# Optimization experiments

Hardware: AMD Instinct MI355X
Metric: run time of the kernel (lower is better)

The kernel has to match this reference:

```python
import jax, jax.numpy as jnp
import numpy as np

B, N, IN_DIM, DIM, KNN = 8, 2048, 128, 128, 16
POS_H = 64
ATTN_H = DIM * 4
EPS = 1e-5
SCALE = 1.0 / np.sqrt(DIM).astype(np.float32)


def setup_inputs() -> dict:
    key = jax.random.key(0)
    ks = jax.random.split(key, 10)
    nrm = lambda k, shape, s=0.02: jax.random.normal(k, shape, jnp.float32) * s
    return dict(
        ori_x=jax.random.normal(ks[0], (B, N, IN_DIM), jnp.float32),
        pos=jax.random.normal(ks[1], (B, N, 3), jnp.float32),
        w_in=nrm(ks[2], (IN_DIM, DIM)),
        w_qkv=nrm(ks[3], (DIM, 3 * DIM)),
        w_out=nrm(ks[4], (DIM, IN_DIM)),
        pos_w1=nrm(ks[5], (3, POS_H)), pos_b1=jnp.zeros((POS_H,), jnp.float32),
        pos_bn_g=jnp.ones((POS_H,), jnp.float32), pos_bn_b=jnp.zeros((POS_H,), jnp.float32),
        pos_bn_m=jnp.zeros((POS_H,), jnp.float32), pos_bn_v=jnp.ones((POS_H,), jnp.float32),
        pos_w2=nrm(ks[6], (POS_H, DIM)), pos_b2=jnp.zeros((DIM,), jnp.float32),
        attn_w1=nrm(ks[7], (DIM, ATTN_H)), attn_b1=jnp.zeros((ATTN_H,), jnp.float32),
        attn_bn_g=jnp.ones((ATTN_H,), jnp.float32), attn_bn_b=jnp.zeros((ATTN_H,), jnp.float32),
        attn_bn_m=jnp.zeros((ATTN_H,), jnp.float32), attn_bn_v=jnp.ones((ATTN_H,), jnp.float32),
        attn_w2=nrm(ks[8], (ATTN_H, DIM)), attn_b2=jnp.zeros((DIM,), jnp.float32),
    )


def _bn_eval(x, g, b, m, v):
    # BatchNorm2d in eval mode; channel is the last axis in our [b,n,k,C] layout
    return (x - m) * (g * jax.lax.rsqrt(v + EPS)) + b


def reference(ori_x, pos, w_in, w_qkv, w_out,
              pos_w1, pos_b1, pos_bn_g, pos_bn_b, pos_bn_m, pos_bn_v, pos_w2, pos_b2,
              attn_w1, attn_b1, attn_bn_g, attn_bn_b, attn_bn_m, attn_bn_v, attn_w2, attn_b2):
    x = ori_x @ w_in                                  # [b,n,dim]
    qkv = x @ w_qkv
    q, k, v = jnp.split(qkv, 3, axis=-1)              # each [b,n,dim]

    # pairwise squared distances [b,n,n] (monotone in rel_dist -> same topk)
    sq = jnp.sum(pos * pos, axis=-1)
    d2 = sq[:, :, None] + sq[:, None, :] - 2.0 * jnp.einsum('bnd,bmd->bnm', pos, pos)
    _, idx = jax.lax.top_k(-d2, KNN)                  # [b,n,KNN] nearest neighbors

    gather = jax.vmap(lambda t, i: t[i])              # [n,C],[n,k] -> [n,k,C] per batch
    k_g = gather(k, idx)                              # [b,n,k,dim]
    v_g = gather(v, idx)
    pos_g = gather(pos, idx)                          # [b,n,k,3]

    rel_pos = pos[:, :, None, :] - pos_g              # [b,n,k,3]
    pe = jax.nn.relu(_bn_eval(rel_pos @ pos_w1 + pos_b1, pos_bn_g, pos_bn_b, pos_bn_m, pos_bn_v))
    pe = pe @ pos_w2 + pos_b2                         # [b,n,k,dim]

    qk_rel = q[:, :, None, :] - k_g                   # [b,n,k,dim]
    h = jax.nn.relu(_bn_eval((qk_rel + pe) @ attn_w1 + attn_b1,
                             attn_bn_g, attn_bn_b, attn_bn_m, attn_bn_v))
    h = h @ attn_w2 + attn_b2                         # [b,n,k,dim]

    attn = jax.nn.softmax(h * SCALE, axis=-2)         # softmax over neighbors
    agg = jnp.sum(attn * (v_g + pe), axis=2)          # [b,n,dim]
    return agg @ w_out + ori_x
```

## Files before the change

kernel.cpp:

```cpp
#include <hip/hip_runtime.h>

#define EPS 1e-5f

constexpr int NB   = 8;
constexpr int NN   = 2048;
constexpr int DIM  = 128;
constexpr int KNN  = 16;
constexpr int AH   = 512;
constexpr int NPTS = NB * NN;
constexpr float SCALE = 0.08838834764831845f;

typedef __attribute__((ext_vector_type(8))) short short8;
typedef __attribute__((ext_vector_type(4))) float floatx4;

__device__ __forceinline__ short f2bf(float f) {
  union { float f; unsigned u; } a; a.f = f;
  return (short)((a.u + 0x8000u) >> 16);
}
__device__ __forceinline__ float bf2f(short s) {
  union { unsigned u; float f; } a; a.u = ((unsigned)(unsigned short)s) << 16;
  return a.f;
}

__global__ __launch_bounds__(256) void gemm_f32(
    const float* __restrict__ A, const float* __restrict__ W,
    float* __restrict__ C, int M, int N, int K)
{
  __shared__ float As[64][33];
  __shared__ float Ws[32][65];
  const int bm = blockIdx.x * 64, bn = blockIdx.y * 64;
  const int tid = threadIdx.x;
  const int tx = tid & 15, ty = tid >> 4;
  float acc[4][4] = {};
  for (int k0 = 0; k0 < K; k0 += 32) {
#pragma unroll
    for (int i = 0; i < 8; ++i) {
      int e = tid + i * 256;
      As[e >> 5][e & 31] = A[(size_t)(bm + (e >> 5)) * K + k0 + (e & 31)];
    }
#pragma unroll
    for (int i = 0; i < 8; ++i) {
      int e = tid + i * 256;
      Ws[e >> 6][e & 63] = W[(size_t)(k0 + (e >> 6)) * N + bn + (e & 63)];
    }
    __syncthreads();
#pragma unroll
    for (int kk = 0; kk < 32; ++kk) {
      float a[4], w[4];
#pragma unroll
      for (int i = 0; i < 4; ++i) a[i] = As[ty * 4 + i][kk];
#pragma unroll
      for (int j = 0; j < 4; ++j) w[j] = Ws[kk][tx * 4 + j];
#pragma unroll
      for (int i = 0; i < 4; ++i)
#pragma unroll
        for (int j = 0; j < 4; ++j)
          acc[i][j] += a[i] * w[j];
    }
    __syncthreads();
  }
#pragma unroll
  for (int i = 0; i < 4; ++i)
#pragma unroll
    for (int j = 0; j < 4; ++j)
      C[(size_t)(bm + ty * 4 + i) * N + bn + tx * 4 + j] = acc[i][j];
}

__global__ __launch_bounds__(256) void knn_kernel(
    const float* __restrict__ pos_t, int* __restrict__ idx_out)
{
  const int tid = threadIdx.x;
  const int lane = tid & 63;
  const int p = blockIdx.x * 4 + (tid >> 6);
  const int b = p >> 11, i = p & (NN - 1);
  const float* px = pos_t + (size_t)b * 3 * NN;
  const float* py = px + NN;
  const float* pz = py + NN;
  const float xi = px[i], yi = py[i], zi = pz[i];
  const float sqi = xi * xi + yi * yi + zi * zi;
  float v[32];
#pragma unroll
  for (int t = 0; t < 32; ++t) {
    int j = t * 64 + lane;
    float xj = px[j], yj = py[j], zj = pz[j];
    float sqj = xj * xj + yj * yj + zj * zj;
    float dot = xi * xj + yi * yj + zi * zj;
    v[t] = sqi + sqj - 2.0f * dot;
  }
  for (int s = 0; s < KNN; ++s) {
    float bv = 3.4e38f; int bj = 1 << 30;
#pragma unroll
    for (int t = 0; t < 32; ++t) {
      if (v[t] < bv) { bv = v[t]; bj = t * 64 + lane; }
    }
#pragma unroll
    for (int m = 1; m < 64; m <<= 1) {
      float ov = __shfl_xor(bv, m);
      int   oj = __shfl_xor(bj, m);
      if (ov < bv || (ov == bv && oj < bj)) { bv = ov; bj = oj; }
    }
    if (lane == 0) idx_out[(size_t)p * KNN + s] = bj;
#pragma unroll
    for (int t = 0; t < 32; ++t)
      if (bj == t * 64 + lane) v[t] = 3.4e38f;
  }
}

__global__ __launch_bounds__(256) void pack_weights(
    const float* __restrict__ attn_w1, const float* __restrict__ attn_w2,
    const float* __restrict__ pos_w2, const float* __restrict__ Wf,
    const float* __restrict__ w_out, const float* __restrict__ pos,
    const float* __restrict__ attn_b1, const float* __restrict__ abn_g,
    const float* __restrict__ abn_b, const float* __restrict__ abn_m,
    const float* __restrict__ abn_v,
    const float* __restrict__ pos_b1, const float* __restrict__ pbn_g,
    const float* __restrict__ pbn_b, const float* __restrict__ pbn_m,
    const float* __restrict__ pbn_v, const float* __restrict__ pos_b2,
    short* __restrict__ w1p, short* __restrict__ w2p, short* __restrict__ pw2p,
    short* __restrict__ wfp, short* __restrict__ wop,
    float* __restrict__ biasq,
    float* __restrict__ t1sc, float* __restrict__ t1bi,
    float* __restrict__ phsc, float* __restrict__ phbi,
    float* __restrict__ pos_t)
{
  int t = blockIdx.x * 256 + threadIdx.x;
  if (t < 65536) {
    int j = t & 7, lane = (t >> 3) & 63, ks = (t >> 9) & 3, nt = (t >> 11) & 3, ch = t >> 13;
    int q = lane >> 4, cc = lane & 15;
    int k = ks * 32 + q * 8 + j, n = ch * 64 + nt * 16 + cc;
    w1p[t] = f2bf(attn_w1[(size_t)k * AH + n]);
  } else if (t < 131072) {
    int e = t - 65536;
    int j = e & 7, lane = (e >> 3) & 63, ks = (e >> 9) & 1, nt = (e >> 10) & 7, ch = e >> 13;
    int q = lane >> 4, cc = lane & 15;
    int k = ch * 64 + ks * 32 + q * 8 + j, n = nt * 16 + cc;
    w2p[e] = f2bf(attn_w2[(size_t)k * DIM + n]);
  } else if (t < 139264) {
    int e = t - 131072;
    int j = e & 7, lane = (e >> 3) & 63, ks = (e >> 9) & 1, nt = e >> 10;
    int q = lane >> 4, cc = lane & 15;
    int k = ks * 32 + q * 8 + j, n = nt * 16 + cc;
    pw2p[e] = f2bf(pos_w2[(size_t)k * DIM + n]);
  } else if (t < 188416) {
    int e = t - 139264;
    int j = e & 7, lane = (e >> 3) & 63, ks = (e >> 9) & 3, nt = (e >> 11) & 7, nc = e >> 14;
    int q = lane >> 4, cc = lane & 15;
    int k = ks * 32 + q * 8 + j, n = nc * 128 + nt * 16 + cc;
    wfp[e] = f2bf(Wf[(size_t)k * 384 + n]);
  } else if (t < 204800) {
    int e = t - 188416;
    int j = e & 7, lane = (e >> 3) & 63, ks = (e >> 9) & 3, nt = (e >> 11) & 7;
    int q = lane >> 4, cc = lane & 15;
    int k = ks * 32 + q * 8 + j, n = nt * 16 + cc;
    wop[e] = f2bf(w_out[(size_t)k * DIM + n]);
  } else if (t < 205184) {
    int c = t - 204800;
    biasq[c] = (c < 128) ? pos_b2[c] : ((c < 256) ? 0.0f : pos_b2[c - 256]);
  } else if (t < 205696) {
    int c = t - 205184;
    t1sc[c] = abn_g[c] * rsqrtf(abn_v[c] + EPS);
  } else if (t < 206208) {
    int c = t - 205696;
    float sc = abn_g[c] * rsqrtf(abn_v[c] + EPS);
    t1bi[c] = (attn_b1[c] - abn_m[c]) * sc + abn_b[c];
  } else if (t < 206272) {
    int c = t - 206208;
    phsc[c] = pbn_g[c] * rsqrtf(pbn_v[c] + EPS);
  } else if (t < 206336) {
    int c = t - 206272;
    float sc = pbn_g[c] * rsqrtf(pbn_v[c] + EPS);
    phbi[c] = (pos_b1[c] - pbn_m[c]) * sc + pbn_b[c];
  } else if (t < 206336 + NPTS * 3) {
    int e = t - 206336;
    int p = e / 3, d = e - p * 3;
    int b = p >> 11, n = p & (NN - 1);
    pos_t[((size_t)b * 3 + d) * NN + n] = pos[e];
  }
}

__global__ __launch_bounds__(256, 4) void gemm_in(
    const float* __restrict__ A, const short* __restrict__ wfp,
    const float* __restrict__ biasq, short* __restrict__ C)
{
  __shared__ short As[64 * 128];
  const int tid = threadIdx.x;
  const int lane = tid & 63, w = tid >> 6;
  const int wr = w >> 1, wc = w & 1;
  const int q = lane >> 4, cc = lane & 15;
  const int row0 = blockIdx.x * 64;
#pragma unroll
  for (int it = 0; it < 4; ++it) {
    int e = tid + it * 256;
    int row = e >> 4, cg = e & 15;
    const float* src = A + (size_t)(row0 + row) * 128 + cg * 8;
    float4 f0 = *(const float4*)src, f1 = *(const float4*)(src + 4);
    short8 v;
    v[0] = f2bf(f0.x); v[1] = f2bf(f0.y); v[2] = f2bf(f0.z); v[3] = f2bf(f0.w);
    v[4] = f2bf(f1.x); v[5] = f2bf(f1.y); v[6] = f2bf(f1.z); v[7] = f2bf(f1.w);
    *(short8*)(As + row * 128 + ((cg ^ (row & 15)) << 3)) = v;
  }
  __syncthreads();
  for (int nc = 0; nc < 3; ++nc) {
    floatx4 acc[2][4];
#pragma unroll
    for (int i = 0; i < 2; ++i)
#pragma unroll
      for (int jt = 0; jt < 4; ++jt) acc[i][jt] = (floatx4){0.f, 0.f, 0.f, 0.f};
#pragma unroll
    for (int ks = 0; ks < 4; ++ks) {
      short8 a8[2], b8[4];
#pragma unroll
      for (int i = 0; i < 2; ++i) {
        int row = (wr * 2 + i) * 16 + cc;
        a8[i] = *(const short8*)(As + row * 128 + (((ks * 4 + q) ^ cc) << 3));
      }
#pragma unroll
      for (int jt = 0; jt < 4; ++jt)
        b8[jt] = *(const short8*)(wfp + ((((nc * 8 + wc * 4 + jt) * 4 + ks) * 64 + lane) << 3));
#pragma unroll
      for (int i = 0; i < 2; ++i)
#pragma unroll
        for (int jt = 0; jt < 4; ++jt)
          acc[i][jt] = __builtin_amdgcn_mfma_f32_16x16x32_bf16(a8[i], b8[jt], acc[i][jt], 0, 0, 0);
    }
#pragma unroll
    for (int jt = 0; jt < 4; ++jt) {
      int colG = nc * 128 + (wc * 4 + jt) * 16 + cc;
      float bv = biasq[colG];
#pragma unroll
      for (int i = 0; i < 2; ++i)
#pragma unroll
        for (int r = 0; r < 4; ++r) {
          int row = (wr * 2 + i) * 16 + q * 4 + r;
          C[(size_t)(row0 + row) * 384 + colG] = f2bf(acc[i][jt][r] + bv);
        }
    }
  }
}

__global__ __launch_bounds__(256, 4) void gemm_out(
    const float* __restrict__ A, const short* __restrict__ wop,
    const float* __restrict__ R, float* __restrict__ C)
{
  __shared__ short As[64 * 128];
  const int tid = threadIdx.x;
  const int lane = tid & 63, w = tid >> 6;
  const int wr = w >> 1, wc = w & 1;
  const int q = lane >> 4, cc = lane & 15;
  const int row0 = blockIdx.x * 64;
#pragma unroll
  for (int it = 0; it < 4; ++it) {
    int e = tid + it * 256;
    int row = e >> 4, cg = e & 15;
    const float* src = A + (size_t)(row0 + row) * 128 + cg * 8;
    float4 f0 = *(const float4*)src, f1 = *(const float4*)(src + 4);
    short8 v;
    v[0] = f2bf(f0.x); v[1] = f2bf(f0.y); v[2] = f2bf(f0.z); v[3] = f2bf(f0.w);
    v[4] = f2bf(f1.x); v[5] = f2bf(f1.y); v[6] = f2bf(f1.z); v[7] = f2bf(f1.w);
    *(short8*)(As + row * 128 + ((cg ^ (row & 15)) << 3)) = v;
  }
  __syncthreads();
  floatx4 acc[2][4];
#pragma unroll
  for (int i = 0; i < 2; ++i)
#pragma unroll
    for (int jt = 0; jt < 4; ++jt) acc[i][jt] = (floatx4){0.f, 0.f, 0.f, 0.f};
#pragma unroll
  for (int ks = 0; ks < 4; ++ks) {
    short8 a8[2], b8[4];
#pragma unroll
    for (int i = 0; i < 2; ++i) {
      int row = (wr * 2 + i) * 16 + cc;
      a8[i] = *(const short8*)(As + row * 128 + (((ks * 4 + q) ^ cc) << 3));
    }
#pragma unroll
    for (int jt = 0; jt < 4; ++jt)
      b8[jt] = *(const short8*)(wop + ((((wc * 4 + jt) * 4 + ks) * 64 + lane) << 3));
#pragma unroll
    for (int i = 0; i < 2; ++i)
#pragma unroll
      for (int jt = 0; jt < 4; ++jt)
        acc[i][jt] = __builtin_amdgcn_mfma_f32_16x16x32_bf16(a8[i], b8[jt], acc[i][jt], 0, 0, 0);
  }
#pragma unroll
  for (int jt = 0; jt < 4; ++jt) {
    int col = (wc * 4 + jt) * 16 + cc;
#pragma unroll
    for (int i = 0; i < 2; ++i)
#pragma unroll
      for (int r = 0; r < 4; ++r) {
        int row = (wr * 2 + i) * 16 + q * 4 + r;
        size_t o = (size_t)(row0 + row) * 128 + col;
        C[o] = acc[i][jt][r] + R[o];
      }
  }
}

__global__ __launch_bounds__(256, 3) void fused_attn(
    const float* __restrict__ pos, const short* __restrict__ qkv,
    const int* __restrict__ knn_idx,
    const float* __restrict__ pos_w1,
    const short* __restrict__ w1p, const short* __restrict__ w2p,
    const short* __restrict__ pw2p,
    const float* __restrict__ t1sc, const float* __restrict__ t1bi,
    const float* __restrict__ phsc, const float* __restrict__ phbi,
    const float* __restrict__ attn_b2,
    float* __restrict__ agg)
{
  __shared__ short a_s[64 * 128];
  __shared__ short vpe_s[64 * 128];
  __shared__ short t1_s[2][64 * 64];
  __shared__ short q_ss[4 * 128];
  __shared__ float relp_s[64 * 4];
  __shared__ int   nbr_s[64];

  const int tid = threadIdx.x;
  const int lane = tid & 63, w = tid >> 6;
  const int wr = w >> 1, wc = w & 1;
  const int q = lane >> 4, cc = lane & 15;
  const int bb = blockIdx.x & 7;
  const int gp0 = bb * NN + (blockIdx.x >> 3) * 4;

  if (tid < 64) nbr_s[tid] = knn_idx[(size_t)gp0 * KNN + tid];
  if (tid >= 64 && tid < 128) {
    int e = tid - 64;
    int p = e >> 4, seg = e & 15;
    *(short8*)(q_ss + p * 128 + seg * 8) =
        *(const short8*)(qkv + (size_t)(gp0 + p) * 384 + seg * 8);
  }
  __syncthreads();
  if (tid < 64) {
    int p = tid >> 4;
    int j = nbr_s[tid];
    const float* pa = pos + (size_t)(gp0 + p) * 3;
    const float* pj = pos + ((size_t)bb * NN + j) * 3;
    relp_s[tid * 4 + 0] = pa[0] - pj[0];
    relp_s[tid * 4 + 1] = pa[1] - pj[1];
    relp_s[tid * 4 + 2] = pa[2] - pj[2];
  }
  __syncthreads();

#pragma unroll
  for (int r2 = 0; r2 < 16; ++r2) {
    int e = tid + r2 * 256;
    int row = e >> 6, c = e & 63;
    float lin = relp_s[row * 4] * pos_w1[c] + relp_s[row * 4 + 1] * pos_w1[64 + c]
              + relp_s[row * 4 + 2] * pos_w1[128 + c];
    t1_s[0][row * 64 + (((c >> 3) ^ (row & 7)) << 3) + (c & 7)] =
        f2bf(fmaxf(lin * phsc[c] + phbi[c], 0.0f));
  }
  __syncthreads();

  floatx4 pe[2][4];
#pragma unroll
  for (int i = 0; i < 2; ++i)
#pragma unroll
    for (int jt = 0; jt < 4; ++jt) pe[i][jt] = (floatx4){0.f, 0.f, 0.f, 0.f};
#pragma unroll
  for (int ks = 0; ks < 2; ++ks) {
    short8 a8[2];
#pragma unroll
    for (int i = 0; i < 2; ++i) {
      int row = (wr * 2 + i) * 16 + cc;
      a8[i] = *(const short8*)(t1_s[0] + row * 64 + (((ks * 4 + q) ^ (row & 7)) << 3));
    }
#pragma unroll
    for (int jt = 0; jt < 4; ++jt) {
      short8 b8 = *(const short8*)(pw2p + ((((wc * 4 + jt) * 2 + ks) * 64 + lane) << 3));
#pragma unroll
      for (int i = 0; i < 2; ++i)
        pe[i][jt] = __builtin_amdgcn_mfma_f32_16x16x32_bf16(a8[i], b8, pe[i][jt], 0, 0, 0);
    }
  }

#pragma unroll
  for (int i = 0; i < 2; ++i) {
    int rt = wr * 2 + i;
#pragma unroll
    for (int jt = 0; jt < 4; ++jt) {
      int col = (wc * 4 + jt) * 16 + cc;
      float qv = bf2f(q_ss[rt * 128 + col]);
#pragma unroll
      for (int r = 0; r < 4; ++r) {
        int row = rt * 16 + q * 4 + r;
        const short* kv = qkv + ((size_t)bb * NN + nbr_s[row]) * 384;
        float pev = pe[i][jt][r];
        int slot = row * 128 + (((col >> 3) ^ (row & 15)) << 3) + (col & 7);
        a_s[slot]   = f2bf(qv - bf2f(kv[128 + col]) + pev);
        vpe_s[slot] = f2bf(bf2f(kv[256 + col]) + pev);
      }
    }
  }
  __syncthreads();

  floatx4 hacc[2][4];
#pragma unroll
  for (int i = 0; i < 2; ++i)
#pragma unroll
    for (int jt = 0; jt < 4; ++jt) hacc[i][jt] = (floatx4){0.f, 0.f, 0.f, 0.f};

  for (int ch = 0; ch < 8; ++ch) {
    short* t1b = t1_s[ch & 1];
    floatx4 tacc[2][2];
#pragma unroll
    for (int i = 0; i < 2; ++i)
#pragma unroll
      for (int jt = 0; jt < 2; ++jt) tacc[i][jt] = (floatx4){0.f, 0.f, 0.f, 0.f};
#pragma unroll
    for (int ks = 0; ks < 4; ++ks) {
      short8 a8[2], b8[2];
#pragma unroll
      for (int i = 0; i < 2; ++i) {
        int row = (wr * 2 + i) * 16 + cc;
        a8[i] = *(const short8*)(a_s + row * 128 + (((ks * 4 + q) ^ cc) << 3));
      }
#pragma unroll
      for (int jt = 0; jt < 2; ++jt)
        b8[jt] = *(const short8*)(w1p + ((((ch * 4 + wc * 2 + jt) * 4 + ks) * 64 + lane) << 3));
#pragma unroll
      for (int i = 0; i < 2; ++i)
#pragma unroll
        for (int jt = 0; jt < 2; ++jt)
          tacc[i][jt] = __builtin_amdgcn_mfma_f32_16x16x32_bf16(a8[i], b8[jt], tacc[i][jt], 0, 0, 0);
    }
#pragma unroll
    for (int jt = 0; jt < 2; ++jt) {
      int colL = (wc * 2 + jt) * 16 + cc;
      int colG = ch * 64 + colL;
      float sc = t1sc[colG], bi = t1bi[colG];
#pragma unroll
      for (int i = 0; i < 2; ++i)
#pragma unroll
        for (int r = 0; r < 4; ++r) {
          int row = (wr * 2 + i) * 16 + q * 4 + r;
          t1b[row * 64 + (((colL >> 3) ^ (row & 7)) << 3) + (colL & 7)] =
              f2bf(fmaxf(tacc[i][jt][r] * sc + bi, 0.0f));
        }
    }
    __syncthreads();
#pragma unroll
    for (int ks = 0; ks < 2; ++ks) {
      short8 a8[2], b8[4];
#pragma unroll
      for (int i = 0; i < 2; ++i) {
        int row = (wr * 2 + i) * 16 + cc;
        a8[i] = *(const short8*)(t1b + row * 64 + (((ks * 4 + q) ^ (row & 7)) << 3));
      }
#pragma unroll
      for (int jt = 0; jt < 4; ++jt)
        b8[jt] = *(const short8*)(w2p + ((((ch * 8 + wc * 4 + jt) * 2 + ks) * 64 + lane) << 3));
#pragma unroll
      for (int i = 0; i < 2; ++i)
#pragma unroll
        for (int jt = 0; jt < 4; ++jt)
          hacc[i][jt] = __builtin_amdgcn_mfma_f32_16x16x32_bf16(a8[i], b8[jt], hacc[i][jt], 0, 0, 0);
    }
  }

#pragma unroll
  for (int i = 0; i < 2; ++i) {
    int rt = wr * 2 + i;
#pragma unroll
    for (int jt = 0; jt < 4; ++jt) {
      int col = (wc * 4 + jt) * 16 + cc;
      float b2v = attn_b2[col];
      float v0[4], mx = -3.4e38f;
#pragma unroll
      for (int r = 0; r < 4; ++r) {
        v0[r] = (hacc[i][jt][r] + b2v) * SCALE;
        mx = fmaxf(mx, v0[r]);
      }
      mx = fmaxf(mx, __shfl_xor(mx, 16));
      mx = fmaxf(mx, __shfl_xor(mx, 32));
      float ex[4], sum = 0.f;
#pragma unroll
      for (int r = 0; r < 4; ++r) { ex[r] = __expf(v0[r] - mx); sum += ex[r]; }
      sum += __shfl_xor(sum, 16);
      sum += __shfl_xor(sum, 32);
      float inv = 1.0f / sum;
      float part = 0.f;
#pragma unroll
      for (int r = 0; r < 4; ++r) {
        int row = rt * 16 + q * 4 + r;
        int slot = row * 128 + (((col >> 3) ^ (row & 15)) << 3) + (col & 7);
        part += ex[r] * bf2f(vpe_s[slot]);
      }
      part += __shfl_xor(part, 16);
      part += __shfl_xor(part, 32);
      if (q == 0) agg[(size_t)(gp0 + rt) * DIM + col] = part * inv;
    }
  }
}

extern "C" void kernel_launch(void* const* d_in, const int* in_sizes, int n_in,
                              void* d_out, int out_size, void* d_ws, size_t ws_size,
                              hipStream_t stream)
{
  const float* ori_x    = (const float*)d_in[0];
  const float* pos      = (const float*)d_in[1];
  const float* w_in     = (const float*)d_in[2];
  const float* w_qkv    = (const float*)d_in[3];
  const float* w_out    = (const float*)d_in[4];
  const float* pos_w1   = (const float*)d_in[5];
  const float* pos_b1   = (const float*)d_in[6];
  const float* pos_bn_g = (const float*)d_in[7];
  const float* pos_bn_b = (const float*)d_in[8];
  const float* pos_bn_m = (const float*)d_in[9];
  const float* pos_bn_v = (const float*)d_in[10];
  const float* pos_w2   = (const float*)d_in[11];
  const float* pos_b2   = (const float*)d_in[12];
  const float* attn_w1  = (const float*)d_in[13];
  const float* attn_b1  = (const float*)d_in[14];
  const float* attn_bn_g = (const float*)d_in[15];
  const float* attn_bn_b = (const float*)d_in[16];
  const float* attn_bn_m = (const float*)d_in[17];
  const float* attn_bn_v = (const float*)d_in[18];
  const float* attn_w2  = (const float*)d_in[19];
  const float* attn_b2  = (const float*)d_in[20];
  float* out = (float*)d_out;

  float* agg  = (float*)d_ws;
  float* Wf   = agg;
  short* qkvb = (short*)(agg + (size_t)NPTS * DIM);
  int*   idx  = (int*)(qkvb + (size_t)NPTS * 3 * DIM);
  short* w1p  = (short*)(idx + (size_t)NPTS * KNN);
  short* w2p  = w1p + 65536;
  short* pw2p = w2p + 65536;
  short* wfp  = pw2p + 8192;
  short* wop  = wfp + 49152;
  float* biasq = (float*)(wop + 16384);
  float* t1sc = biasq + 384;
  float* t1bi = t1sc + 512;
  float* phsc = t1bi + 512;
  float* phbi = phsc + 64;
  float* pos_t = phbi + 64;

  gemm_f32<<<dim3(2, 6), 256, 0, stream>>>(w_in, w_qkv, Wf, 128, 384, 128);
  pack_weights<<<998, 256, 0, stream>>>(attn_w1, attn_w2, pos_w2, Wf, w_out, pos,
      attn_b1, attn_bn_g, attn_bn_b, attn_bn_m, attn_bn_v,
      pos_b1, pos_bn_g, pos_bn_b, pos_bn_m, pos_bn_v, pos_b2,
      w1p, w2p, pw2p, wfp, wop, biasq, t1sc, t1bi, phsc, phbi, pos_t);
  gemm_in<<<NPTS / 64, 256, 0, stream>>>(ori_x, wfp, biasq, qkvb);
  knn_kernel<<<NPTS / 4, 256, 0, stream>>>(pos_t, idx);
  fused_attn<<<NPTS / 4, 256, 0, stream>>>(pos, qkvb, idx, pos_w1,
      w1p, w2p, pw2p, t1sc, t1bi, phsc, phbi, attn_b2, agg);
  gemm_out<<<NPTS / 64, 256, 0, stream>>>(agg, wop, ori_x, out);
}
```

Measured before the change: 361.5 us.

## Give each wave its own point to remove block barriers in fused attention

Restructures fused_attn so each of the four waves owns one query point (16 neighbor rows) end to end. This removes every __syncthreads and leaves only wave-private shared-memory buffers. The A-operand fragments are held in registers across all hidden-layer chunks, and the shared buffer is reused for v+pe. Shared memory drops from roughly 52KB to about 25KB. In exchange each wave now loads every weight B-fragment itself instead of splitting columns across waves, which doubles global/L2 weight traffic per block and adds register pressure.

```diff
diff --git a/kernel.cpp b/kernel.cpp
--- a/kernel.cpp
+++ b/kernel.cpp
@@ -307,188 +307,163 @@
     const float* __restrict__ attn_b2,
     float* __restrict__ agg)
 {
-  __shared__ short a_s[64 * 128];
-  __shared__ short vpe_s[64 * 128];
-  __shared__ short t1_s[2][64 * 64];
-  __shared__ short q_ss[4 * 128];
-  __shared__ float relp_s[64 * 4];
-  __shared__ int   nbr_s[64];
+  __shared__ short av_s[64 * 128];
+  __shared__ short t1p[4][16 * 64];
+  __shared__ float relp_s[4][64];
+  __shared__ int   nbr_s[4][16];
 
   const int tid = threadIdx.x;
   const int lane = tid & 63, w = tid >> 6;
-  const int wr = w >> 1, wc = w & 1;
   const int q = lane >> 4, cc = lane & 15;
   const int bb = blockIdx.x & 7;
   const int gp0 = bb * NN + (blockIdx.x >> 3) * 4;
-
-  if (tid < 64) nbr_s[tid] = knn_idx[(size_t)gp0 * KNN + tid];
-  if (tid >= 64 && tid < 128) {
-    int e = tid - 64;
-    int p = e >> 4, seg = e & 15;
-    *(short8*)(q_ss + p * 128 + seg * 8) =
-        *(const short8*)(qkv + (size_t)(gp0 + p) * 384 + seg * 8);
-  }
-  __syncthreads();
-  if (tid < 64) {
-    int p = tid >> 4;
-    int j = nbr_s[tid];
-    const float* pa = pos + (size_t)(gp0 + p) * 3;
-    const float* pj = pos + ((size_t)bb * NN + j) * 3;
-    relp_s[tid * 4 + 0] = pa[0] - pj[0];
-    relp_s[tid * 4 + 1] = pa[1] - pj[1];
-    relp_s[tid * 4 + 2] = pa[2] - pj[2];
-  }
-  __syncthreads();
-
-#pragma unroll
-  for (int r2 = 0; r2 < 16; ++r2) {
-    int e = tid + r2 * 256;
-    int row = e >> 6, c = e & 63;
-    float lin = relp_s[row * 4] * pos_w1[c] + relp_s[row * 4 + 1] * pos_w1[64 + c]
-              + relp_s[row * 4 + 2] * pos_w1[128 + c];
-    t1_s[0][row * 64 + (((c >> 3) ^ (row & 7)) << 3) + (c & 7)] =
-        f2bf(fmaxf(lin * phsc[c] + phbi[c], 0.0f));
-  }
-  __syncthreads();
-
-  floatx4 pe[2][4];
-#pragma unroll
-  for (int i = 0; i < 2; ++i)
-#pragma unroll
-    for (int jt = 0; jt < 4; ++jt) pe[i][jt] = (floatx4){0.f, 0.f, 0.f, 0.f};
+  const int pt = gp0 + w;
+
+  if (lane < 16) {
+    int nbr = knn_idx[(size_t)pt * KNN + lane];
+    nbr_s[w][lane] = nbr;
+    const float* pa = pos + (size_t)pt * 3;
+    const float* pj = pos + ((size_t)bb * NN + nbr) * 3;
+    relp_s[w][lane * 4 + 0] = pa[0] - pj[0];
+    relp_s[w][lane * 4 + 1] = pa[1] - pj[1];
+    relp_s[w][lane * 4 + 2] = pa[2] - pj[2];
+  }
+
+  short* t1w = t1p[w];
+
+  {
+    const int c = lane;
+    float w1x = pos_w1[c], w1y = pos_w1[64 + c], w1z = pos_w1[128 + c];
+    float sc = phsc[c], bi = phbi[c];
+#pragma unroll
+    for (int r = 0; r < 16; ++r) {
+      float lin = relp_s[w][r * 4] * w1x + relp_s[w][r * 4 + 1] * w1y
+                + relp_s[w][r * 4 + 2] * w1z;
+      t1w[r * 64 + (((c >> 3) ^ (r & 7)) << 3) + (c & 7)] =
+          f2bf(fmaxf(lin * sc + bi, 0.0f));
+    }
+  }
+
+  floatx4 pe[8];
+#pragma unroll
+  for (int jt = 0; jt < 8; ++jt) pe[jt] = (floatx4){0.f, 0.f, 0.f, 0.f};
 #pragma unroll
   for (int ks = 0; ks < 2; ++ks) {
-    short8 a8[2];
-#pragma unroll
-    for (int i = 0; i < 2; ++i) {
-      int row = (wr * 2 + i) * 16 + cc;
-      a8[i] = *(const short8*)(t1_s[0] + row * 64 + (((ks * 4 + q) ^ (row & 7)) << 3));
+    short8 a8 = *(const short8*)(t1w + cc * 64 + (((ks * 4 + q) ^ (cc & 7)) << 3));
+#pragma unroll
+    for (int jt = 0; jt < 8; ++jt) {
+      short8 b8 = *(const short8*)(pw2p + (((jt * 2 + ks) * 64 + lane) << 3));
+      pe[jt] = __builtin_amdgcn_mfma_f32_16x16x32_bf16(a8, b8, pe[jt], 0, 0, 0);
+    }
+  }
+
+  float qreg[8];
+#pragma unroll
+  for (int jt = 0; jt < 8; ++jt)
+    qreg[jt] = bf2f(qkv[(size_t)pt * 384 + jt * 16 + cc]);
+
+  floatx4 vpe[8];
+#pragma unroll
+  for (int r = 0; r < 4; ++r) {
+    int lr = q * 4 + r;
+    int row = w * 16 + lr;
+    const short* kv = qkv + ((size_t)bb * NN + nbr_s[w][lr]) * 384;
+    int sb = row * 128;
+#pragma unroll
+    for (int jt = 0; jt < 8; ++jt) {
+      int col = jt * 16 + cc;
+      float pev = pe[jt][r];
+      av_s[sb + (((col >> 3) ^ lr) << 3) + (col & 7)] =
+          f2bf(qreg[jt] - bf2f(kv[128 + col]) + pev);
+      vpe[jt][r] = bf2f(kv[256 + col]) + pev;
+    }
+  }
+
+  short8 af[4];
+#pragma unroll
+  for (int ks = 0; ks < 4; ++ks)
+    af[ks] = *(const short8*)(av_s + (w * 16 + cc) * 128 + (((ks * 4 + q) ^ cc) << 3));
+
+#pragma unroll
+  for (int r = 0; r < 4; ++r) {
+    int lr = q * 4 + r;
+    int sb = (w * 16 + lr) * 128;
+#pragma unroll
+    for (int jt = 0; jt < 8; ++jt) {
+      int col = jt * 16 + cc;
+      av_s[sb + (((col >> 3) ^ lr) << 3) + (col & 7)] = f2bf(vpe[jt][r]);
+    }
+  }
+
+  floatx4 hacc[8];
+#pragma unroll
+  for (int jt = 0; jt < 8; ++jt) hacc[jt] = (floatx4){0.f, 0.f, 0.f, 0.f};
+
+  for (int ch = 0; ch < 8; ++ch) {
+    floatx4 tacc[4];
+#pragma unroll
+    for (int jt = 0; jt < 4; ++jt) tacc[jt] = (floatx4){0.f, 0.f, 0.f, 0.f};
+#pragma unroll
+    for (int ks = 0; ks < 4; ++ks) {
+      short8 b8[4];
+#pragma unroll
+      for (int jt = 0; jt < 4; ++jt)
+        b8[jt] = *(const short8*)(w1p + ((((ch * 4 + jt) * 4 + ks) * 64 + lane) << 3));
+#pragma unroll
+      for (int jt = 0; jt < 4; ++jt)
+        tacc[jt] = __builtin_amdgcn_mfma_f32_16x16x32_bf16(af[ks], b8[jt], tacc[jt], 0, 0, 0);
     }
 #pragma unroll
     for (int jt = 0; jt < 4; ++jt) {
-      short8 b8 = *(const short8*)(pw2p + ((((wc * 4 + jt) * 2 + ks) * 64 + lane) << 3));
-#pragma unroll
-      for (int i = 0; i < 2; ++i)
-        pe[i][jt] = __builtin_amdgcn_mfma_f32_16x16x32_bf16(a8[i], b8, pe[i][jt], 0, 0, 0);
-    }
-  }
-
-#pragma unroll
-  for (int i = 0; i < 2; ++i) {
-    int rt = wr * 2 + i;
-#pragma unroll
-    for (int jt = 0; jt < 4; ++jt) {
-      int col = (wc * 4 + jt) * 16 + cc;
-      float qv = bf2f(q_ss[rt * 128 + col]);
-#pragma unroll
-      for (int r = 0; r < 4; ++r) {
-        int row = rt * 16 + q * 4 + r;
-        const short* kv = qkv + ((size_t)bb * NN + nbr_s[row]) * 384;
-        float pev = pe[i][jt][r];
-        int slot = row * 128 + (((col >> 3) ^ (row & 15)) << 3) + (col & 7);
-        a_s[slot]   = f2bf(qv - bf2f(kv[128 + col]) + pev);
-        vpe_s[slot] = f2bf(bf2f(kv[256 + col]) + pev);
-      }
-    }
-  }
-  __syncthreads();
-
-  floatx4 hacc[2][4];
-#pragma unroll
-  for (int i = 0; i < 2; ++i)
-#pragma unroll
-    for (int jt = 0; jt < 4; ++jt) hacc[i][jt] = (floatx4){0.f, 0.f, 0.f, 0.f};
-
-  for (int ch = 0; ch < 8; ++ch) {
-    short* t1b = t1_s[ch & 1];
-    floatx4 tacc[2][2];
-#pragma unroll
-    for (int i = 0; i < 2; ++i)
-#pragma unroll
-      for (int jt = 0; jt < 2; ++jt) tacc[i][jt] = (floatx4){0.f, 0.f, 0.f, 0.f};
-#pragma unroll
-    for (int ks = 0; ks < 4; ++ks) {
-      short8 a8[2], b8[2];
-#pragma unroll
-      for (int i = 0; i < 2; ++i) {
-        int row = (wr * 2 + i) * 16 + cc;
-        a8[i] = *(const short8*)(a_s + row * 128 + (((ks * 4 + q) ^ cc) << 3));
-      }
-#pragma unroll
-      for (int jt = 0; jt < 2; ++jt)
-        b8[jt] = *(const short8*)(w1p + ((((ch * 4 + wc * 2 + jt) * 4 + ks) * 64 + lane) << 3));
-#pragma unroll
-      for (int i = 0; i < 2; ++i)
-#pragma unroll
-        for (int jt = 0; jt < 2; ++jt)
-          tacc[i][jt] = __builtin_amdgcn_mfma_f32_16x16x32_bf16(a8[i], b8[jt], tacc[i][jt], 0, 0, 0);
-    }
-#pragma unroll
-    for (int jt = 0; jt < 2; ++jt) {
-      int colL = (wc * 2 + jt) * 16 + cc;
+      int colL = jt * 16 + cc;
       int colG = ch * 64 + colL;
       float sc = t1sc[colG], bi = t1bi[colG];
 #pragma unroll
-      for (int i = 0; i < 2; ++i)
-#pragma unroll
-        for (int r = 0; r < 4; ++r) {
-          int row = (wr * 2 + i) * 16 + q * 4 + r;
-          t1b[row * 64 + (((colL >> 3) ^ (row & 7)) << 3) + (colL & 7)] =
-              f2bf(fmaxf(tacc[i][jt][r] * sc + bi, 0.0f));
-        }
-    }
-    __syncthreads();
+      for (int r = 0; r < 4; ++r) {
+        int lr = q * 4 + r;
+        t1w[lr * 64 + (((colL >> 3) ^ (lr & 7)) << 3) + (colL & 7)] =
+            f2bf(fmaxf(tacc[jt][r] * sc + bi, 0.0f));
+      }
+    }
 #pragma unroll
     for (int ks = 0; ks < 2; ++ks) {
-      short8 a8[2], b8[4];
-#pragma unroll
-      for (int i = 0; i < 2; ++i) {
-        int row = (wr * 2 + i) * 16 + cc;
-        a8[i] = *(const short8*)(t1b + row * 64 + (((ks * 4 + q) ^ (row & 7)) << 3));
+      short8 a8 = *(const short8*)(t1w + cc * 64 + (((ks * 4 + q) ^ (cc & 7)) << 3));
+#pragma unroll
+      for (int jt = 0; jt < 8; ++jt) {
+        short8 b8 = *(const short8*)(w2p + ((((ch * 8 + jt) * 2 + ks) * 64 + lane) << 3));
+        hacc[jt] = __builtin_amdgcn_mfma_f32_16x16x32_bf16(a8, b8, hacc[jt], 0, 0, 0);
       }
-#pragma unroll
-      for (int jt = 0; jt < 4; ++jt)
-        b8[jt] = *(const short8*)(w2p + ((((ch * 8 + wc * 4 + jt) * 2 + ks) * 64 + lane) << 3));
-#pragma unroll
-      for (int i = 0; i < 2; ++i)
-#pragma unroll
-        for (int jt = 0; jt < 4; ++jt)
-          hacc[i][jt] = __builtin_amdgcn_mfma_f32_16x16x32_bf16(a8[i], b8[jt], hacc[i][jt], 0, 0, 0);
-    }
-  }
-
-#pragma unroll
-  for (int i = 0; i < 2; ++i) {
-    int rt = wr * 2 + i;
-#pragma unroll
-    for (int jt = 0; jt < 4; ++jt) {
-      int col = (wc * 4 + jt) * 16 + cc;
-      float b2v = attn_b2[col];
-      float v0[4], mx = -3.4e38f;
-#pragma unroll
-      for (int r = 0; r < 4; ++r) {
-        v0[r] = (hacc[i][jt][r] + b2v) * SCALE;
-        mx = fmaxf(mx, v0[r]);
-      }
-      mx = fmaxf(mx, __shfl_xor(mx, 16));
-      mx = fmaxf(mx, __shfl_xor(mx, 32));
-      float ex[4], sum = 0.f;
-#pragma unroll
-      for (int r = 0; r < 4; ++r) { ex[r] = __expf(v0[r] - mx); sum += ex[r]; }
-      sum += __shfl_xor(sum, 16);
-      sum += __shfl_xor(sum, 32);
-      float inv = 1.0f / sum;
-      float part = 0.f;
-#pragma unroll
-      for (int r = 0; r < 4; ++r) {
-        int row = rt * 16 + q * 4 + r;
-        int slot = row * 128 + (((col >> 3) ^ (row & 15)) << 3) + (col & 7);
-        part += ex[r] * bf2f(vpe_s[slot]);
-      }
-      part += __shfl_xor(part, 16);
-      part += __shfl_xor(part, 32);
-      if (q == 0) agg[(size_t)(gp0 + rt) * DIM + col] = part * inv;
-    }
+    }
+  }
+
+#pragma unroll
+  for (int jt = 0; jt < 8; ++jt) {
+    int col = jt * 16 + cc;
+    float b2v = attn_b2[col];
+    float v0[4], mx = -3.4e38f;
+#pragma unroll
+    for (int r = 0; r < 4; ++r) {
+      v0[r] = (hacc[jt][r] + b2v) * SCALE;
+      mx = fmaxf(mx, v0[r]);
+    }
+    mx = fmaxf(mx, __shfl_xor(mx, 16));
+    mx = fmaxf(mx, __shfl_xor(mx, 32));
+    float ex[4], sum = 0.f;
+#pragma unroll
+    for (int r = 0; r < 4; ++r) { ex[r] = __expf(v0[r] - mx); sum += ex[r]; }
+    sum += __shfl_xor(sum, 16);
+    sum += __shfl_xor(sum, 32);
+    float inv = 1.0f / sum;
+    float part = 0.f;
+#pragma unroll
+    for (int r = 0; r < 4; ++r) {
+      int lr = q * 4 + r;
+      int slot = (w * 16 + lr) * 128 + (((col >> 3) ^ lr) << 3) + (col & 7);
+      part += ex[r] * bf2f(av_s[slot]);
+    }
+    part += __shfl_xor(part, 16);
+    part += __shfl_xor(part, 32);
+    if (q == 0) agg[(size_t)pt * DIM + col] = part * inv;
   }
 }
 
```

Result: slower. 416.3 us (+15.2%).
